# Kernel tuning notes

Hardware: AMD Instinct MI355X
Metric: run time of the kernel (lower is better)

## Reference

```python
import jax, jax.numpy as jnp
import numpy as np

N, D, H, O, E = 4096, 1024, 4096, 1024, 8
TOP_K = 2

def setup_inputs() -> dict:
    key = jax.random.key(0)
    k = jax.random.split(key, 4)
    x  = jax.random.normal(k[0], (N, D), dtype=jnp.float32)
    Wg = jax.random.normal(k[1], (D, E), dtype=jnp.float32) * (1.0 / np.sqrt(D))
    W1 = jax.random.normal(k[2], (E, D, H), dtype=jnp.float32) * (1.0 / np.sqrt(D))
    b1 = jnp.zeros((E, H), dtype=jnp.float32)
    W2 = jax.random.normal(k[3], (E, H, O), dtype=jnp.float32) * (1.0 / np.sqrt(H))
    b2 = jnp.zeros((E, O), dtype=jnp.float32)
    return {"x": x, "Wg": Wg, "W1": W1, "b1": b1, "W2": W2, "b2": b2}

def reference(x, Wg, W1, b1, W2, b2):
    # Gate: Linear(bias=False) -> ReLU (lin() appends act) -> softmax
    logits = jax.nn.relu(x @ Wg)                      # [N, E]
    probs = jax.nn.softmax(logits, axis=1)            # [N, E]
    top_p, sel = jax.lax.top_k(probs, TOP_K)          # [N, K]
    top_p = top_p / jnp.sum(top_p, axis=-1, keepdims=True)
    # Per-token combine weights over experts: [N, E]
    combine = jnp.sum(jax.nn.one_hot(sel, E, dtype=x.dtype) * top_p[..., None], axis=1)
    # Experts: ReLU(x W1 + b1) -> ReLU(h W2 + b2); final ReLU because lin() adds act on output layer
    h = jax.nn.relu(jnp.einsum('nd,edh->enh', x, W1) + b1[:, None, :])   # [E, N, H]
    y = jax.nn.relu(jnp.einsum('enh,eho->eno', h, W2) + b2[:, None, :])  # [E, N, O]
    out = jnp.einsum('eno,ne->no', y, combine)                            # [N, O]
    return out
```

## Files before the change

kernel.cpp:

```cpp
#include <hip/hip_runtime.h>
#include <cstdint>

#define NTOK 4096
#define DDIM 1024
#define HDIM 4096
#define ODIM 1024
#define NEXP 8
#define NSLOT (2*NTOK)
#define MAXTILES 72

typedef __bf16 bf16x8 __attribute__((ext_vector_type(8)));
typedef float  f32x4  __attribute__((ext_vector_type(4)));
typedef unsigned short ushort8v __attribute__((ext_vector_type(8)));

__device__ __forceinline__ unsigned short f2bf(float f) {
    union { float f; unsigned int u; } v; v.f = f;
    unsigned int r = (v.u + 0x7FFF + ((v.u >> 16) & 1)) >> 16;
    return (unsigned short)r;
}

typedef const void __attribute__((address_space(1)))* gas_ptr;
typedef void       __attribute__((address_space(3)))* las_ptr;

__global__ void gate_kernel(const float* __restrict__ x, const float* __restrict__ Wg,
                            int2* __restrict__ sel, float2* __restrict__ wts,
                            int* __restrict__ counts, unsigned short* __restrict__ xb) {
    int wave = threadIdx.x >> 6;
    int lane = threadIdx.x & 63;
    int n = blockIdx.x * 4 + wave;
    float acc[NEXP];
#pragma unroll
    for (int e = 0; e < NEXP; e++) acc[e] = 0.f;
    const float* xr = x + (size_t)n * DDIM;
    unsigned short* xbr = xb + (size_t)n * DDIM;
    for (int i = 0; i < DDIM / 64; i++) {
        int d = i * 64 + lane;
        float xv = xr[d];
        xbr[d] = f2bf(xv);
        const float* wr = Wg + d * NEXP;
#pragma unroll
        for (int e = 0; e < NEXP; e++) acc[e] = fmaf(xv, wr[e], acc[e]);
    }
#pragma unroll
    for (int e = 0; e < NEXP; e++) {
#pragma unroll
        for (int off = 32; off >= 1; off >>= 1)
            acc[e] += __shfl_xor(acc[e], off, 64);
    }
    if (lane == 0) {
        float l0 = -1e30f, l1 = -1e30f; int e0 = 0, e1 = 0;
#pragma unroll
        for (int e = 0; e < NEXP; e++) {
            float v = fmaxf(acc[e], 0.f);
            if (v > l0)      { l1 = l0; e1 = e0; l0 = v; e0 = e; }
            else if (v > l1) { l1 = v;  e1 = e; }
        }
        float w0 = 1.f / (1.f + expf(l1 - l0));
        sel[n] = make_int2(e0, e1);
        wts[n] = make_float2(w0, 1.f - w0);
        atomicAdd(&counts[e0], 1);
        atomicAdd(&counts[e1], 1);
    }
}

__global__ void route_kernel(const int2* __restrict__ sel, const float2* __restrict__ wts,
                             const int* __restrict__ counts, int* __restrict__ offsets,
                             int4* __restrict__ tile_meta, int* __restrict__ ntiles,
                             int* __restrict__ slot_token, float* __restrict__ slot_weight) {
    __shared__ int cur[NEXP];
    int t = threadIdx.x;
    if (t == 0) {
        int s = 0, nt = 0;
        for (int e = 0; e < NEXP; e++) {
            offsets[e] = s; cur[e] = s;
            int c = counts[e];
            for (int r = 0; r < c; r += 128)
                tile_meta[nt++] = make_int4(e, s + r, min(128, c - r), 0);
            s += c;
        }
        offsets[NEXP] = s;
        *ntiles = nt;
    }
    __syncthreads();
    for (int n = t; n < NTOK; n += blockDim.x) {
        int2 se = sel[n]; float2 w = wts[n];
        int p0 = atomicAdd(&cur[se.x], 1);
        slot_token[p0] = n; slot_weight[p0] = w.x;
        int p1 = atomicAdd(&cur[se.y], 1);
        slot_token[p1] = n; slot_weight[p1] = w.y;
    }
}

__global__ void transpose_cast_kernel(const float* __restrict__ src, unsigned short* __restrict__ dst,
                                      int R, int C) {
    __shared__ float tile[64][65];
    int e = blockIdx.z;
    const float* s = src + (size_t)e * R * C;
    unsigned short* d = dst + (size_t)e * R * C;
    int t = threadIdx.x;
    int r0 = blockIdx.y * 64, c0 = blockIdx.x * 64;
#pragma unroll
    for (int p = 0; p < 4; p++) {
        int r = p * 16 + (t >> 4);
        int c = (t & 15) * 4;
        float4 v = *(const float4*)&s[(size_t)(r0 + r) * C + (c0 + c)];
        tile[r][c] = v.x; tile[r][c + 1] = v.y; tile[r][c + 2] = v.z; tile[r][c + 3] = v.w;
    }
    __syncthreads();
    int c = t >> 2, rb = (t & 3) * 16;
#pragma unroll
    for (int j = 0; j < 2; j++) {
        ushort8v v;
#pragma unroll
        for (int i = 0; i < 8; i++) v[i] = f2bf(tile[rb + j * 8 + i][c]);
        *(ushort8v*)&d[(size_t)(c0 + c) * R + (r0 + rb + j * 8)] = v;
    }
}

template <int MODE, int KDIM, int NDIM>
__global__ __launch_bounds__(256) void moe_gemm_kernel(
    const unsigned short* __restrict__ A,
    const unsigned short* __restrict__ B,
    const float* __restrict__ bias,
    const int4* __restrict__ tile_meta,
    const int* __restrict__ ntiles,
    const int* __restrict__ slot_token,
    const float* __restrict__ slot_weight,
    unsigned short* __restrict__ h,
    float* __restrict__ out) {

    if ((int)blockIdx.y >= *ntiles) return;
    int4 tm = tile_meta[blockIdx.y];
    int e = tm.x, slotBase = tm.y, rows = tm.z;
    int colBase = blockIdx.x * 128;

    __shared__ __align__(16) unsigned short As[2][128 * 64];
    __shared__ __align__(16) unsigned short Bs[2][128 * 64];

    int tid = threadIdx.x;
    int w = tid >> 6, l = tid & 63;
    int quad = l >> 4, lr = l & 15;
    int wm = w & 1, wn = w >> 1;
    int lr8 = l >> 3, u = l & 7;
    int gu = u ^ lr8;

    const unsigned short* ag[4];
    const unsigned short* bg[4];
    const unsigned short* Be = B + (size_t)e * NDIM * KDIM;
#pragma unroll
    for (int j = 0; j < 4; j++) {
        int r = 32 * w + 8 * j + lr8;
        int slot = min(slotBase + r, NSLOT - 1);
        if constexpr (MODE == 1) {
            int tok = slot_token[slot];
            ag[j] = A + (size_t)tok * KDIM + gu * 8;
        } else {
            ag[j] = A + (size_t)slot * KDIM + gu * 8;
        }
        bg[j] = Be + (size_t)(colBase + r) * KDIM + gu * 8;
    }

    f32x4 zero = {0.f, 0.f, 0.f, 0.f};
    f32x4 acc[4][4];
#pragma unroll
    for (int m = 0; m < 4; m++)
#pragma unroll
        for (int n = 0; n < 4; n++) acc[m][n] = zero;

    int swz = (lr & 7);
    constexpr int NI = KDIM / 64;

    auto issue = [&](int k, int s) {
        unsigned short* AsW = &As[s][32 * w * 64];
        unsigned short* BsW = &Bs[s][32 * w * 64];
#pragma unroll
        for (int j = 0; j < 4; j++)
            __builtin_amdgcn_global_load_lds((gas_ptr)(ag[j] + k * 64), (las_ptr)(AsW + j * 512), 16, 0, 0);
#pragma unroll
        for (int j = 0; j < 4; j++)
            __builtin_amdgcn_global_load_lds((gas_ptr)(bg[j] + k * 64), (las_ptr)(BsW + j * 512), 16, 0, 0);
    };
    auto compute = [&](int s) {
        const unsigned short* A_ = As[s];
        const unsigned short* B_ = Bs[s];
#pragma unroll
        for (int ks = 0; ks < 2; ks++) {
            int su = ((ks * 4 + quad) ^ swz) * 8;
            bf16x8 af[4], bf[4];
#pragma unroll
            for (int m = 0; m < 4; m++)
                af[m] = *(const bf16x8*)&A_[(wm * 64 + m * 16 + lr) * 64 + su];
#pragma unroll
            for (int n = 0; n < 4; n++)
                bf[n] = *(const bf16x8*)&B_[(wn * 64 + n * 16 + lr) * 64 + su];
#pragma unroll
            for (int m = 0; m < 4; m++)
#pragma unroll
                for (int n = 0; n < 4; n++)
                    acc[m][n] = __builtin_amdgcn_mfma_f32_16x16x32_bf16(af[m], bf[n], acc[m][n], 0, 0, 0);
        }
    };

    issue(0, 0);
    for (int k = 0; k < NI - 1; k++) {
        issue(k + 1, (k + 1) & 1);
        asm volatile("s_waitcnt vmcnt(8)" ::: "memory");
        asm volatile("s_barrier" ::: "memory");
        compute(k & 1);
        asm volatile("s_barrier" ::: "memory");
    }
    asm volatile("s_waitcnt vmcnt(0)" ::: "memory");
    asm volatile("s_barrier" ::: "memory");
    compute((NI - 1) & 1);

    if constexpr (MODE == 1) {
        const float* bv = bias + e * NDIM;
#pragma unroll
        for (int n = 0; n < 4; n++) {
            int gc = colBase + wn * 64 + n * 16 + lr;
            float b = bv[gc];
#pragma unroll
            for (int m = 0; m < 4; m++) {
                int rloc = wm * 64 + m * 16 + quad * 4;
#pragma unroll
                for (int i = 0; i < 4; i++) {
                    int r = rloc + i;
                    if (r < rows) {
                        float v = fmaxf(acc[m][n][i] + b, 0.f);
                        h[(size_t)(slotBase + r) * NDIM + gc] = f2bf(v);
                    }
                }
            }
        }
    } else {
        const float* bv = bias + e * NDIM;
#pragma unroll
        for (int m = 0; m < 4; m++) {
            int rloc = wm * 64 + m * 16 + quad * 4;
#pragma unroll
            for (int i = 0; i < 4; i++) {
                int r = rloc + i;
                if (r >= rows) continue;
                int s = slotBase + r;
                int tok = slot_token[s];
                float wgt = slot_weight[s];
                float* orow = out + (size_t)tok * ODIM;
#pragma unroll
                for (int n = 0; n < 4; n++) {
                    int gc = colBase + wn * 64 + n * 16 + lr;
                    float v = fmaxf(acc[m][n][i] + bv[gc], 0.f) * wgt;
                    atomicAdd(&orow[gc], v);
                }
            }
        }
    }
}

extern "C" void kernel_launch(void* const* d_in, const int* in_sizes, int n_in,
                              void* d_out, int out_size, void* d_ws, size_t ws_size,
                              hipStream_t stream) {
    const float* x  = (const float*)d_in[0];
    const float* Wg = (const float*)d_in[1];
    const float* W1 = (const float*)d_in[2];
    const float* b1 = (const float*)d_in[3];
    const float* W2 = (const float*)d_in[4];
    const float* b2 = (const float*)d_in[5];
    float* out = (float*)d_out;

    char* ws = (char*)d_ws;
    int*    counts      = (int*)(ws + 0);
    int*    offsets     = (int*)(ws + 128);
    int*    ntiles      = (int*)(ws + 192);
    int4*   tile_meta   = (int4*)(ws + 256);
    int2*   sel         = (int2*)(ws + 2048);
    float2* wts         = (float2*)(ws + 34816);
    int*    slot_token  = (int*)(ws + 67584);
    float*  slot_weight = (float*)(ws + 100352);
    unsigned short* xb  = (unsigned short*)(ws + 2097152);
    unsigned short* W1T = (unsigned short*)(ws + 10485760);
    unsigned short* W2T = (unsigned short*)(ws + 77594624);
    unsigned short* hbf = (unsigned short*)(ws + 144703488);

    hipMemsetAsync(d_out, 0, (size_t)NTOK * ODIM * sizeof(float), stream);
    hipMemsetAsync(ws, 0, 256, stream);

    gate_kernel<<<NTOK / 4, 256, 0, stream>>>(x, Wg, sel, wts, counts, xb);
    route_kernel<<<1, 512, 0, stream>>>(sel, wts, counts, offsets, tile_meta, ntiles,
                                        slot_token, slot_weight);

    transpose_cast_kernel<<<dim3(HDIM / 64, DDIM / 64, NEXP), 256, 0, stream>>>(W1, W1T, DDIM, HDIM);
    transpose_cast_kernel<<<dim3(ODIM / 64, HDIM / 64, NEXP), 256, 0, stream>>>(W2, W2T, HDIM, ODIM);

    moe_gemm_kernel<1, DDIM, HDIM><<<dim3(HDIM / 128, MAXTILES), 256, 0, stream>>>(
        xb, W1T, b1, tile_meta, ntiles, slot_token, slot_weight, hbf, nullptr);
    moe_gemm_kernel<2, HDIM, ODIM><<<dim3(ODIM / 128, MAXTILES), 256, 0, stream>>>(
        hbf, W2T, b2, tile_meta, ntiles, slot_token, slot_weight, nullptr, out);
}
```

Measured before the change: 775.3 us.

## Use larger asymmetric MoE GEMM tiles with K=32 stages and vectorized gate

Makes the expert GEMM kernel a template over tile shape. The first GEMM now uses 128x256 tiles, and the second uses 256-row tiles from a separate 256-row tile list, with a remapped grid so blocks sharing a row tile run close together. Each pipeline stage now loads a 32-wide K slice with a new LDS swizzle, each wave keeps an 8x4 MFMA accumulator block, and launch bounds now request 2 blocks per CU. The gate kernel also switches to float4 loads. The aim is more operand reuse per loaded byte and fewer blocks. The cost is higher register pressure, shallower K stages with more barriers, and more wasted rows in partially filled 256-row tiles.

```diff
diff --git a/kernel.cpp b/kernel.cpp
--- a/kernel.cpp
+++ b/kernel.cpp
@@ -7,7 +7,8 @@
 #define ODIM 1024
 #define NEXP 8
 #define NSLOT (2*NTOK)
-#define MAXTILES 72
+#define MAXT128 72
+#define MAXT256 40
 
 typedef __bf16 bf16x8 __attribute__((ext_vector_type(8)));
 typedef float  f32x4  __attribute__((ext_vector_type(4)));
@@ -33,13 +34,21 @@
     for (int e = 0; e < NEXP; e++) acc[e] = 0.f;
     const float* xr = x + (size_t)n * DDIM;
     unsigned short* xbr = xb + (size_t)n * DDIM;
-    for (int i = 0; i < DDIM / 64; i++) {
-        int d = i * 64 + lane;
-        float xv = xr[d];
-        xbr[d] = f2bf(xv);
-        const float* wr = Wg + d * NEXP;
-#pragma unroll
-        for (int e = 0; e < NEXP; e++) acc[e] = fmaf(xv, wr[e], acc[e]);
+#pragma unroll
+    for (int i = 0; i < 4; i++) {
+        int d = i * 256 + lane * 4;
+        float4 xv = *(const float4*)&xr[d];
+        ushort4 o;
+        o.x = f2bf(xv.x); o.y = f2bf(xv.y); o.z = f2bf(xv.z); o.w = f2bf(xv.w);
+        *(ushort4*)&xbr[d] = o;
+        const float* wr = Wg + (size_t)d * NEXP;
+#pragma unroll
+        for (int jj = 0; jj < 4; jj++) {
+            float xs = (jj == 0) ? xv.x : (jj == 1) ? xv.y : (jj == 2) ? xv.z : xv.w;
+#pragma unroll
+            for (int e = 0; e < NEXP; e++)
+                acc[e] = fmaf(xs, wr[jj * NEXP + e], acc[e]);
+        }
     }
 #pragma unroll
     for (int e = 0; e < NEXP; e++) {
@@ -65,21 +74,24 @@
 
 __global__ void route_kernel(const int2* __restrict__ sel, const float2* __restrict__ wts,
                              const int* __restrict__ counts, int* __restrict__ offsets,
-                             int4* __restrict__ tile_meta, int* __restrict__ ntiles,
+                             int4* __restrict__ t128, int* __restrict__ nt128,
+                             int4* __restrict__ t256, int* __restrict__ nt256,
                              int* __restrict__ slot_token, float* __restrict__ slot_weight) {
     __shared__ int cur[NEXP];
     int t = threadIdx.x;
     if (t == 0) {
-        int s = 0, nt = 0;
+        int s = 0, n1 = 0, n2 = 0;
         for (int e = 0; e < NEXP; e++) {
             offsets[e] = s; cur[e] = s;
             int c = counts[e];
             for (int r = 0; r < c; r += 128)
-                tile_meta[nt++] = make_int4(e, s + r, min(128, c - r), 0);
+                t128[n1++] = make_int4(e, s + r, min(128, c - r), 0);
+            for (int r = 0; r < c; r += 256)
+                t256[n2++] = make_int4(e, s + r, min(256, c - r), 0);
             s += c;
         }
         offsets[NEXP] = s;
-        *ntiles = nt;
+        *nt128 = n1; *nt256 = n2;
     }
     __syncthreads();
     for (int n = t; n < NTOK; n += blockDim.x) {
@@ -117,8 +129,8 @@
     }
 }
 
-template <int MODE, int KDIM, int NDIM>
-__global__ __launch_bounds__(256) void moe_gemm_kernel(
+template <int MODE, int KDIM, int NDIM, int TM, int TN, int WMv>
+__global__ __launch_bounds__(256, 2) void moe_gemm_kernel(
     const unsigned short* __restrict__ A,
     const unsigned short* __restrict__ B,
     const float* __restrict__ bias,
@@ -129,82 +141,94 @@
     unsigned short* __restrict__ h,
     float* __restrict__ out) {
 
-    if ((int)blockIdx.y >= *ntiles) return;
-    int4 tm = tile_meta[blockIdx.y];
+    int tileIdx, colBase;
+    if constexpr (MODE == 1) {
+        tileIdx = blockIdx.y;
+        colBase = blockIdx.x * TN;
+    } else {
+        int j = blockIdx.y;
+        tileIdx = blockIdx.x + 8 * (j >> 3);
+        colBase = (j & 7) * TN;
+    }
+    if (tileIdx >= *ntiles) return;
+    int4 tm = tile_meta[tileIdx];
     int e = tm.x, slotBase = tm.y, rows = tm.z;
-    int colBase = blockIdx.x * 128;
-
-    __shared__ __align__(16) unsigned short As[2][128 * 64];
-    __shared__ __align__(16) unsigned short Bs[2][128 * 64];
+
+    constexpr int RA = TM / 4, IA = RA / 16;
+    constexpr int RB = TN / 4, IB = RB / 16;
+    constexpr int NI = KDIM / 32;
+
+    __shared__ __align__(16) unsigned short As[2][TM * 32];
+    __shared__ __align__(16) unsigned short Bs[2][TN * 32];
 
     int tid = threadIdx.x;
     int w = tid >> 6, l = tid & 63;
     int quad = l >> 4, lr = l & 15;
-    int wm = w & 1, wn = w >> 1;
-    int lr8 = l >> 3, u = l & 7;
-    int gu = u ^ lr8;
-
-    const unsigned short* ag[4];
-    const unsigned short* bg[4];
+    int wm = w % WMv, wn = w / WMv;
+
+    int rl = l >> 2;
+    int g = (l & 3) ^ ((l >> 3) & 3);
+
+    const unsigned short* ag[IA];
+    const unsigned short* bg[IB];
     const unsigned short* Be = B + (size_t)e * NDIM * KDIM;
 #pragma unroll
-    for (int j = 0; j < 4; j++) {
-        int r = 32 * w + 8 * j + lr8;
+    for (int j = 0; j < IA; j++) {
+        int r = w * RA + j * 16 + rl;
         int slot = min(slotBase + r, NSLOT - 1);
         if constexpr (MODE == 1) {
             int tok = slot_token[slot];
-            ag[j] = A + (size_t)tok * KDIM + gu * 8;
+            ag[j] = A + (size_t)tok * KDIM + g * 8;
         } else {
-            ag[j] = A + (size_t)slot * KDIM + gu * 8;
-        }
-        bg[j] = Be + (size_t)(colBase + r) * KDIM + gu * 8;
+            ag[j] = A + (size_t)slot * KDIM + g * 8;
+        }
+    }
+#pragma unroll
+    for (int j = 0; j < IB; j++) {
+        int r = w * RB + j * 16 + rl;
+        bg[j] = Be + (size_t)(colBase + r) * KDIM + g * 8;
     }
 
     f32x4 zero = {0.f, 0.f, 0.f, 0.f};
-    f32x4 acc[4][4];
-#pragma unroll
-    for (int m = 0; m < 4; m++)
+    f32x4 acc[8][4];
+#pragma unroll
+    for (int m = 0; m < 8; m++)
 #pragma unroll
         for (int n = 0; n < 4; n++) acc[m][n] = zero;
 
-    int swz = (lr & 7);
-    constexpr int NI = KDIM / 64;
+    int su = (quad ^ ((lr >> 1) & 3)) * 16;
 
     auto issue = [&](int k, int s) {
-        unsigned short* AsW = &As[s][32 * w * 64];
-        unsigned short* BsW = &Bs[s][32 * w * 64];
-#pragma unroll
-        for (int j = 0; j < 4; j++)
-            __builtin_amdgcn_global_load_lds((gas_ptr)(ag[j] + k * 64), (las_ptr)(AsW + j * 512), 16, 0, 0);
-#pragma unroll
-        for (int j = 0; j < 4; j++)
-            __builtin_amdgcn_global_load_lds((gas_ptr)(bg[j] + k * 64), (las_ptr)(BsW + j * 512), 16, 0, 0);
+        unsigned short* AsW = &As[s][w * RA * 32];
+        unsigned short* BsW = &Bs[s][w * RB * 32];
+#pragma unroll
+        for (int j = 0; j < IA; j++)
+            __builtin_amdgcn_global_load_lds((gas_ptr)(ag[j] + k * 32), (las_ptr)(AsW + j * 512), 16, 0, 0);
+#pragma unroll
+        for (int j = 0; j < IB; j++)
+            __builtin_amdgcn_global_load_lds((gas_ptr)(bg[j] + k * 32), (las_ptr)(BsW + j * 512), 16, 0, 0);
     };
     auto compute = [&](int s) {
-        const unsigned short* A_ = As[s];
-        const unsigned short* B_ = Bs[s];
-#pragma unroll
-        for (int ks = 0; ks < 2; ks++) {
-            int su = ((ks * 4 + quad) ^ swz) * 8;
-            bf16x8 af[4], bf[4];
-#pragma unroll
-            for (int m = 0; m < 4; m++)
-                af[m] = *(const bf16x8*)&A_[(wm * 64 + m * 16 + lr) * 64 + su];
+        const char* A_ = (const char*)As[s];
+        const char* B_ = (const char*)Bs[s];
+        bf16x8 af[8], bf[4];
+#pragma unroll
+        for (int m = 0; m < 8; m++)
+            af[m] = *(const bf16x8*)(A_ + (wm * 128 + m * 16 + lr) * 64 + su);
+#pragma unroll
+        for (int n = 0; n < 4; n++)
+            bf[n] = *(const bf16x8*)(B_ + (wn * 64 + n * 16 + lr) * 64 + su);
+#pragma unroll
+        for (int m = 0; m < 8; m++)
 #pragma unroll
             for (int n = 0; n < 4; n++)
-                bf[n] = *(const bf16x8*)&B_[(wn * 64 + n * 16 + lr) * 64 + su];
-#pragma unroll
-            for (int m = 0; m < 4; m++)
-#pragma unroll
-                for (int n = 0; n < 4; n++)
-                    acc[m][n] = __builtin_amdgcn_mfma_f32_16x16x32_bf16(af[m], bf[n], acc[m][n], 0, 0, 0);
-        }
+                acc[m][n] = __builtin_amdgcn_mfma_f32_16x16x32_bf16(af[m], bf[n], acc[m][n], 0, 0, 0);
     };
 
     issue(0, 0);
     for (int k = 0; k < NI - 1; k++) {
         issue(k + 1, (k + 1) & 1);
-        asm volatile("s_waitcnt vmcnt(8)" ::: "memory");
+        asm volatile("s_waitcnt vmcnt(6)" ::: "memory");
         asm volatile("s_barrier" ::: "memory");
         compute(k & 1);
         asm volatile("s_barrier" ::: "memory");
@@ -220,8 +244,8 @@
             int gc = colBase + wn * 64 + n * 16 + lr;
             float b = bv[gc];
 #pragma unroll
-            for (int m = 0; m < 4; m++) {
-                int rloc = wm * 64 + m * 16 + quad * 4;
+            for (int m = 0; m < 8; m++) {
+                int rloc = wm * 128 + m * 16 + quad * 4;
 #pragma unroll
                 for (int i = 0; i < 4; i++) {
                     int r = rloc + i;
@@ -235,8 +259,8 @@
     } else {
         const float* bv = bias + e * NDIM;
 #pragma unroll
-        for (int m = 0; m < 4; m++) {
-            int rloc = wm * 64 + m * 16 + quad * 4;
+        for (int m = 0; m < 8; m++) {
+            int rloc = wm * 128 + m * 16 + quad * 4;
 #pragma unroll
             for (int i = 0; i < 4; i++) {
                 int r = rloc + i;
@@ -269,13 +293,15 @@
 
     char* ws = (char*)d_ws;
     int*    counts      = (int*)(ws + 0);
-    int*    offsets     = (int*)(ws + 128);
-    int*    ntiles      = (int*)(ws + 192);
-    int4*   tile_meta   = (int4*)(ws + 256);
-    int2*   sel         = (int2*)(ws + 2048);
-    float2* wts         = (float2*)(ws + 34816);
-    int*    slot_token  = (int*)(ws + 67584);
-    float*  slot_weight = (float*)(ws + 100352);
+    int*    offsets     = (int*)(ws + 64);
+    int*    nt128       = (int*)(ws + 128);
+    int*    nt256       = (int*)(ws + 132);
+    int4*   t128        = (int4*)(ws + 256);
+    int4*   t256        = (int4*)(ws + 2048);
+    int2*   sel         = (int2*)(ws + 4096);
+    float2* wts         = (float2*)(ws + 36864);
+    int*    slot_token  = (int*)(ws + 69632);
+    float*  slot_weight = (float*)(ws + 102400);
     unsigned short* xb  = (unsigned short*)(ws + 2097152);
     unsigned short* W1T = (unsigned short*)(ws + 10485760);
     unsigned short* W2T = (unsigned short*)(ws + 77594624);
@@ -285,14 +311,14 @@
     hipMemsetAsync(ws, 0, 256, stream);
 
     gate_kernel<<<NTOK / 4, 256, 0, stream>>>(x, Wg, sel, wts, counts, xb);
-    route_kernel<<<1, 512, 0, stream>>>(sel, wts, counts, offsets, tile_meta, ntiles,
+    route_kernel<<<1, 512, 0, stream>>>(sel, wts, counts, offsets, t128, nt128, t256, nt256,
                                         slot_token, slot_weight);
 
     transpose_cast_kernel<<<dim3(HDIM / 64, DDIM / 64, NEXP), 256, 0, stream>>>(W1, W1T, DDIM, HDIM);
     transpose_cast_kernel<<<dim3(ODIM / 64, HDIM / 64, NEXP), 256, 0, stream>>>(W2, W2T, HDIM, ODIM);
 
-    moe_gemm_kernel<1, DDIM, HDIM><<<dim3(HDIM / 128, MAXTILES), 256, 0, stream>>>(
-        xb, W1T, b1, tile_meta, ntiles, slot_token, slot_weight, hbf, nullptr);
-    moe_gemm_kernel<2, HDIM, ODIM><<<dim3(ODIM / 128, MAXTILES), 256, 0, stream>>>(
-        hbf, W2T, b2, tile_meta, ntiles, slot_token, slot_weight, nullptr, out);
-}
+    moe_gemm_kernel<1, DDIM, HDIM, 128, 256, 1><<<dim3(HDIM / 256, MAXT128), 256, 0, stream>>>(
+        xb, W1T, b1, t128, nt128, slot_token, slot_weight, hbf, nullptr);
+    moe_gemm_kernel<2, HDIM, ODIM, 256, 128, 2><<<dim3(8, MAXT256), 256, 0, stream>>>(
+        hbf, W2T, b2, t256, nt256, slot_token, slot_weight, nullptr, out);
+}
```

Result: no change. 773.1 us (-0.3%).
